# Optimization experiments

Measured on AMD Instinct MI355X. Metric: run time of the kernel, lower is better.

The kernel has to match this reference:

```python
import jax, jax.numpy as jnp
import numpy as np

B, LQ, LD, H, C = 128, 32, 512, 768, 128


def setup_inputs() -> dict:
    key = jax.random.key(0)
    ks = jax.random.split(key, 8)
    return {
        "query_hidden": jax.random.normal(ks[0], (B, LQ, H), dtype=jnp.float32),
        "doc_hidden": jax.random.normal(ks[1], (B, LD, H), dtype=jnp.float32),
        "query_mask": jax.random.randint(ks[2], (B, LQ), 0, 2, dtype=jnp.int32),
        "doc_mask": jax.random.randint(ks[3], (B, LD), 0, 2, dtype=jnp.int32),
        "W_comp": jax.random.normal(ks[4], (H, C), dtype=jnp.float32) * (1.0 / np.sqrt(H)),
        "b_comp": jax.random.normal(ks[5], (C,), dtype=jnp.float32) * 0.02,
        "w_stop": jax.random.normal(ks[6], (C, 1), dtype=jnp.float32) * (1.0 / np.sqrt(C)),
        "b_stop": jnp.ones((1,), dtype=jnp.float32),  # nn.init.constant_(bias, 1)
        "score_merger": jnp.zeros((1,), dtype=jnp.float32),
    }


def reference(query_hidden, doc_hidden, query_mask, doc_mask,
              W_comp, b_comp, w_stop, b_stop, score_merger):
    qm = query_mask.astype(bool)  # [B, LQ]
    dm = doc_mask.astype(bool)    # [B, LD]

    # encode_shared: CLS vec is the UNcompressed hidden state at position 0
    q_cls = query_hidden[:, 0, :]  # [B, H]
    d_cls = doc_hidden[:, 0, :]    # [B, H]

    # compressor (Linear H->C)
    q_vecs = jnp.einsum('blh,hc->blc', query_hidden, W_comp) + b_comp  # [B, LQ, C]
    d_tok = jnp.einsum('blh,hc->blc', doc_hidden, W_comp) + b_comp     # [B, LD, C]

    # encode_query: zero masked query tokens
    q_vecs = q_vecs * qm[..., None]

    # encode_doc: stopword reducer (relu of Linear C->1), then importance + mask
    importance = jax.nn.relu(jnp.einsum('blc,co->blo', d_tok, w_stop) + b_stop)  # [B, LD, 1]
    d_vecs = d_tok * importance * dm[..., None]

    # CLS score: dot product of (uncompressed) CLS vectors
    cls_score = jnp.sum(q_cls * d_cls, axis=-1)  # [B]

    # term score: MaxSim over doc tokens, masked sum over query tokens
    scores = jnp.einsum('bqc,bkc->bqk', q_vecs, d_vecs)      # [B, LQ, LD]
    scores = jnp.where(dm[:, None, :], scores, -1000.0)
    term = jnp.max(scores, axis=-1)                          # [B, LQ]
    term_score = jnp.sum(jnp.where(qm, term, 0.0), axis=-1)  # [B]

    w = jax.nn.sigmoid(score_merger[0])
    cls_score = cls_score * w
    term_score = term_score * (1.0 - w)
    score = cls_score + term_score
    return (score, cls_score, term_score)
```

## Files before the change

### kernel.cpp

```cpp
#include <hip/hip_runtime.h>
#include <hip/hip_bf16.h>

#define Bb 128
#define LQ 32
#define LD 512
#define Hh 768
#define Cc 128

#define QBLOCKS ((Bb * LQ) / 64)
#define DBLOCKS ((Bb * LD) / 64)

typedef short bf16x8 __attribute__((ext_vector_type(8)));
typedef float f32x4 __attribute__((ext_vector_type(4)));

__device__ __forceinline__ short f2bf(float f) {
  union { float f; unsigned u; } v;
  v.f = f;
  unsigned u = v.u + (0x7FFFu + ((v.u >> 16) & 1u));
  return (short)(u >> 16);
}

__device__ __forceinline__ void pack8(bf16x8& d, const float4& lo, const float4& hi) {
  d[0] = f2bf(lo.x); d[1] = f2bf(lo.y); d[2] = f2bf(lo.z); d[3] = f2bf(lo.w);
  d[4] = f2bf(hi.x); d[5] = f2bf(hi.y); d[6] = f2bf(hi.z); d[7] = f2bf(hi.w);
}

__global__ __launch_bounds__(256) void k_wt(const float* __restrict__ W,
                                            short* __restrict__ Wt) {
  int idx = blockIdx.x * 256 + threadIdx.x;
  int h = idx >> 7;
  int c = idx & 127;
  Wt[c * Hh + h] = f2bf(W[idx]);
}

__global__ __launch_bounds__(256) void k_proj_all(
    const float* __restrict__ qh, const float* __restrict__ dh,
    const short* __restrict__ Wt, const float* __restrict__ bcomp,
    const int* __restrict__ qmask, const int* __restrict__ dmask,
    const float* __restrict__ wstop, const float* __restrict__ bstop,
    float* __restrict__ qv, float* __restrict__ dv) {
  const int tid = threadIdx.x;
  const int wave = tid >> 6;
  const int lane = tid & 63;
  const int quad = lane >> 4;
  const int lm = lane & 15;

  const int blk = blockIdx.x;
  const bool is_doc = blk < DBLOCKS;
  const float* X;
  float* Y;
  const int* mask;
  long row0;
  if (is_doc) {
    X = dh; Y = dv; mask = dmask;
    row0 = (long)blk * 64 + wave * 16;
  } else {
    X = qh; Y = qv; mask = qmask;
    row0 = (long)(blk - DBLOCKS) * 64 + wave * 16;
  }

  const float* pa = X + (row0 + lm) * (long)Hh + quad * 8;
  const short* pb = Wt + lm * Hh + quad * 8;

  f32x4 acc[8];
#pragma unroll
  for (int j = 0; j < 8; ++j) acc[j] = (f32x4){0.f, 0.f, 0.f, 0.f};

  float4 c0 = *(const float4*)(pa);
  float4 c1 = *(const float4*)(pa + 4);
  float4 c2 = *(const float4*)(pa + 32);
  float4 c3 = *(const float4*)(pa + 36);

  for (int kk = 0; kk < Hh; kk += 64) {
    int kn = kk + 64;
    if (kn >= Hh) kn = 0;
    float4 n0 = *(const float4*)(pa + kn);
    float4 n1 = *(const float4*)(pa + kn + 4);
    float4 n2 = *(const float4*)(pa + kn + 32);
    float4 n3 = *(const float4*)(pa + kn + 36);

    bf16x8 fa;
    pack8(fa, c0, c1);
#pragma unroll
    for (int j = 0; j < 8; ++j) {
      bf16x8 fb = *(const bf16x8*)(pb + j * 16 * Hh + kk);
      acc[j] = __builtin_amdgcn_mfma_f32_16x16x32_bf16(fa, fb, acc[j], 0, 0, 0);
    }
    pack8(fa, c2, c3);
#pragma unroll
    for (int j = 0; j < 8; ++j) {
      bf16x8 fb = *(const bf16x8*)(pb + j * 16 * Hh + kk + 32);
      acc[j] = __builtin_amdgcn_mfma_f32_16x16x32_bf16(fa, fb, acc[j], 0, 0, 0);
    }
    c0 = n0; c1 = n1; c2 = n2; c3 = n3;
  }

  float bc[8], wsv[8];
#pragma unroll
  for (int j = 0; j < 8; ++j) bc[j] = bcomp[j * 16 + lm];
  if (is_doc) {
#pragma unroll
    for (int j = 0; j < 8; ++j) wsv[j] = wstop[j * 16 + lm];
  }
  const float bs = is_doc ? bstop[0] : 0.f;

#pragma unroll
  for (int r = 0; r < 4; ++r) {
    const long row = row0 + quad * 4 + r;
    float v[8];
#pragma unroll
    for (int j = 0; j < 8; ++j) v[j] = acc[j][r] + bc[j];
    float scale;
    if (is_doc) {
      float p = 0.f;
#pragma unroll
      for (int j = 0; j < 8; ++j) p += v[j] * wsv[j];
      p += __shfl_xor(p, 1);
      p += __shfl_xor(p, 2);
      p += __shfl_xor(p, 4);
      p += __shfl_xor(p, 8);
      float imp = fmaxf(p + bs, 0.f);
      scale = imp * (float)mask[row];
    } else {
      scale = (float)mask[row];
    }
    float* yr = Y + row * Cc;
#pragma unroll
    for (int j = 0; j < 8; ++j) yr[j * 16 + lm] = v[j] * scale;
  }
}

__global__ __launch_bounds__(256) void k_scores(
    const float* __restrict__ Qv, const float* __restrict__ Dv,
    const int* __restrict__ dmask, float* __restrict__ partial) {
  const int chunk = blockIdx.x;
  const int b = blockIdx.y;
  const int tid = threadIdx.x;
  __shared__ float lq[LQ][Cc + 4];
  __shared__ float ldv[64][Cc + 4];
  __shared__ float pm[LQ][16];
  __shared__ int dmsk[64];

  {
    const float4* src = (const float4*)(Qv + (size_t)b * LQ * Cc);
    for (int i = tid; i < LQ * Cc / 4; i += 256) {
      float4 v = src[i];
      int q = i >> 5;
      int c = (i & 31) << 2;
      *(float4*)&lq[q][c] = v;
    }
  }
  const int k0 = chunk * 64;
  {
    const float4* src = (const float4*)(Dv + ((size_t)b * LD + k0) * Cc);
    for (int i = tid; i < 64 * Cc / 4; i += 256) {
      float4 v = src[i];
      int k = i >> 5;
      int c = (i & 31) << 2;
      *(float4*)&ldv[k][c] = v;
    }
  }
  if (tid < 64) dmsk[tid] = dmask[(size_t)b * LD + k0 + tid];
  __syncthreads();

  const int qt = tid & 15;
  const int kt = tid >> 4;
  const int kbase = kt * 4;
  float a[2][4];
#pragma unroll
  for (int qi = 0; qi < 2; ++qi)
#pragma unroll
    for (int ki = 0; ki < 4; ++ki) a[qi][ki] = 0.f;

  for (int c = 0; c < Cc; c += 4) {
    float4 q0 = *(float4*)&lq[qt][c];
    float4 q1 = *(float4*)&lq[qt + 16][c];
    float4 d0 = *(float4*)&ldv[kbase + 0][c];
    float4 d1 = *(float4*)&ldv[kbase + 1][c];
    float4 d2 = *(float4*)&ldv[kbase + 2][c];
    float4 d3 = *(float4*)&ldv[kbase + 3][c];
    a[0][0] += q0.x * d0.x + q0.y * d0.y + q0.z * d0.z + q0.w * d0.w;
    a[0][1] += q0.x * d1.x + q0.y * d1.y + q0.z * d1.z + q0.w * d1.w;
    a[0][2] += q0.x * d2.x + q0.y * d2.y + q0.z * d2.z + q0.w * d2.w;
    a[0][3] += q0.x * d3.x + q0.y * d3.y + q0.z * d3.z + q0.w * d3.w;
    a[1][0] += q1.x * d0.x + q1.y * d0.y + q1.z * d0.z + q1.w * d0.w;
    a[1][1] += q1.x * d1.x + q1.y * d1.y + q1.z * d1.z + q1.w * d1.w;
    a[1][2] += q1.x * d2.x + q1.y * d2.y + q1.z * d2.z + q1.w * d2.w;
    a[1][3] += q1.x * d3.x + q1.y * d3.y + q1.z * d3.z + q1.w * d3.w;
  }
  float m0 = -1000.f, m1 = -1000.f;
#pragma unroll
  for (int ki = 0; ki < 4; ++ki) {
    if (dmsk[kbase + ki]) {
      m0 = fmaxf(m0, a[0][ki]);
      m1 = fmaxf(m1, a[1][ki]);
    }
  }
  pm[qt][kt] = m0;
  pm[qt + 16][kt] = m1;
  __syncthreads();
  if (tid < LQ) {
    float mx = pm[tid][0];
#pragma unroll
    for (int t = 1; t < 16; ++t) mx = fmaxf(mx, pm[tid][t]);
    partial[((size_t)b * LQ + tid) * 8 + chunk] = mx;
  }
}

__global__ __launch_bounds__(256) void k_final(
    const float* __restrict__ qh, const float* __restrict__ dh,
    const int* __restrict__ qmask, const float* __restrict__ partial,
    const float* __restrict__ merger, float* __restrict__ out) {
  const int b = blockIdx.x;
  const int tid = threadIdx.x;
  __shared__ float red[256];
  __shared__ float clss;
  const float* qc = qh + (size_t)b * LQ * Hh;
  const float* dc = dh + (size_t)b * LD * Hh;
  float s = 0.f;
  for (int h = tid; h < Hh; h += 256) s += qc[h] * dc[h];
  red[tid] = s;
  __syncthreads();
  for (int off = 128; off > 0; off >>= 1) {
    if (tid < off) red[tid] += red[tid + off];
    __syncthreads();
  }
  if (tid == 0) clss = red[0];
  __syncthreads();
  float t = 0.f;
  if (tid < LQ) {
    const float* pp = partial + ((size_t)b * LQ + tid) * 8;
    float mx = pp[0];
#pragma unroll
    for (int c = 1; c < 8; ++c) mx = fmaxf(mx, pp[c]);
    if (qmask[b * LQ + tid]) t = mx;
  }
  red[tid] = t;
  __syncthreads();
  for (int off = 128; off > 0; off >>= 1) {
    if (tid < off) red[tid] += red[tid + off];
    __syncthreads();
  }
  if (tid == 0) {
    float w = 1.f / (1.f + expf(-merger[0]));
    float cs = clss * w;
    float ts = red[0] * (1.f - w);
    out[b] = cs + ts;
    out[Bb + b] = cs;
    out[2 * Bb + b] = ts;
  }
}

extern "C" void kernel_launch(void* const* d_in, const int* in_sizes, int n_in,
                              void* d_out, int out_size, void* d_ws, size_t ws_size,
                              hipStream_t stream) {
  const float* qh  = (const float*)d_in[0];
  const float* dh  = (const float*)d_in[1];
  const int*   qm  = (const int*)d_in[2];
  const int*   dm  = (const int*)d_in[3];
  const float* W   = (const float*)d_in[4];
  const float* bc  = (const float*)d_in[5];
  const float* wst = (const float*)d_in[6];
  const float* bst = (const float*)d_in[7];
  const float* mrg = (const float*)d_in[8];
  float* out = (float*)d_out;

  char* ws = (char*)d_ws;
  short* Wt  = (short*)ws;
  float* qv  = (float*)(ws + 196608);
  float* dv  = (float*)(ws + 196608 + 2097152);
  float* prt = (float*)(ws + 196608 + 2097152 + 33554432);

  k_wt<<<(Hh * Cc) / 256, 256, 0, stream>>>(W, Wt);
  k_proj_all<<<DBLOCKS + QBLOCKS, 256, 0, stream>>>(qh, dh, Wt, bc, qm, dm,
                                                    wst, bst, qv, dv);
  k_scores<<<dim3(8, Bb), 256, 0, stream>>>(qv, dv, dm, prt);
  k_final<<<Bb, 256, 0, stream>>>(qh, dh, qm, prt, mrg, out);
}
```

Baseline: 395.8 us.

## Stage projection A and B tiles through LDS via direct global-to-LDS loads

```diff
diff --git a/kernel.cpp b/kernel.cpp
--- a/kernel.cpp
+++ b/kernel.cpp
@@ -23,6 +23,12 @@
 __device__ __forceinline__ void pack8(bf16x8& d, const float4& lo, const float4& hi) {
   d[0] = f2bf(lo.x); d[1] = f2bf(lo.y); d[2] = f2bf(lo.z); d[3] = f2bf(lo.w);
   d[4] = f2bf(hi.x); d[5] = f2bf(hi.y); d[6] = f2bf(hi.z); d[7] = f2bf(hi.w);
+}
+
+__device__ __forceinline__ void gload16(const void* g, void* l) {
+  __builtin_amdgcn_global_load_lds(
+      (const __attribute__((address_space(1))) void*)g,
+      (__attribute__((address_space(3))) void*)l, 16, 0, 0);
 }
 
 __global__ __launch_bounds__(256) void k_wt(const float* __restrict__ W,
@@ -39,6 +45,9 @@
     const int* __restrict__ qmask, const int* __restrict__ dmask,
     const float* __restrict__ wstop, const float* __restrict__ bstop,
     float* __restrict__ qv, float* __restrict__ dv) {
+  __shared__ float lA[64 * 64];
+  __shared__ short lB[128 * 64];
+
   const int tid = threadIdx.x;
   const int wave = tid >> 6;
   const int lane = tid & 63;
@@ -50,51 +59,61 @@
   const float* X;
   float* Y;
   const int* mask;
-  long row0;
+  long row0b;
   if (is_doc) {
     X = dh; Y = dv; mask = dmask;
-    row0 = (long)blk * 64 + wave * 16;
+    row0b = (long)blk * 64;
   } else {
     X = qh; Y = qv; mask = qmask;
-    row0 = (long)(blk - DBLOCKS) * 64 + wave * 16;
-  }
-
-  const float* pa = X + (row0 + lm) * (long)Hh + quad * 8;
-  const short* pb = Wt + lm * Hh + quad * 8;
+    row0b = (long)(blk - DBLOCKS) * 64;
+  }
 
   f32x4 acc[8];
 #pragma unroll
   for (int j = 0; j < 8; ++j) acc[j] = (f32x4){0.f, 0.f, 0.f, 0.f};
 
-  float4 c0 = *(const float4*)(pa);
-  float4 c1 = *(const float4*)(pa + 4);
-  float4 c2 = *(const float4*)(pa + 32);
-  float4 c3 = *(const float4*)(pa + 36);
+  const int ubase = wave * 256 + lane;
 
   for (int kk = 0; kk < Hh; kk += 64) {
-    int kn = kk + 64;
-    if (kn >= Hh) kn = 0;
-    float4 n0 = *(const float4*)(pa + kn);
-    float4 n1 = *(const float4*)(pa + kn + 4);
-    float4 n2 = *(const float4*)(pa + kn + 32);
-    float4 n3 = *(const float4*)(pa + kn + 36);
-
-    bf16x8 fa;
-    pack8(fa, c0, c1);
-#pragma unroll
-    for (int j = 0; j < 8; ++j) {
-      bf16x8 fb = *(const bf16x8*)(pb + j * 16 * Hh + kk);
-      acc[j] = __builtin_amdgcn_mfma_f32_16x16x32_bf16(fa, fb, acc[j], 0, 0, 0);
-    }
-    pack8(fa, c2, c3);
-#pragma unroll
-    for (int j = 0; j < 8; ++j) {
-      bf16x8 fb = *(const bf16x8*)(pb + j * 16 * Hh + kk + 32);
-      acc[j] = __builtin_amdgcn_mfma_f32_16x16x32_bf16(fa, fb, acc[j], 0, 0, 0);
-    }
-    c0 = n0; c1 = n1; c2 = n2; c3 = n3;
-  }
-
+#pragma unroll
+    for (int i = 0; i < 4; ++i) {
+      int u = ubase + i * 64;
+      int r = u >> 4, s = u & 15;
+      int g = s ^ (r & 7);
+      gload16(X + (row0b + r) * (long)Hh + kk + g * 4,
+              &lA[(wave * 4 + i) * 256]);
+    }
+#pragma unroll
+    for (int i = 0; i < 4; ++i) {
+      int u = ubase + i * 64;
+      int n = u >> 3, s = u & 7;
+      int g = s ^ (n & 7);
+      gload16(Wt + n * Hh + kk + g * 8,
+              &lB[(wave * 4 + i) * 512]);
+    }
+    __syncthreads();
+
+    const int rr = wave * 16 + lm;
+#pragma unroll
+    for (int h = 0; h < 2; ++h) {
+      const int gf = h * 8 + quad * 2;
+      const int s0 = gf ^ (lm & 7);
+      const int s1 = (gf + 1) ^ (lm & 7);
+      float4 a0 = *(const float4*)&lA[rr * 64 + s0 * 4];
+      float4 a1 = *(const float4*)&lA[rr * 64 + s1 * 4];
+      bf16x8 fa;
+      pack8(fa, a0, a1);
+      const int sb = (h * 4 + quad) ^ (lm & 7);
+#pragma unroll
+      for (int j = 0; j < 8; ++j) {
+        bf16x8 fb = *(const bf16x8*)&lB[(j * 16 + lm) * 64 + sb * 8];
+        acc[j] = __builtin_amdgcn_mfma_f32_16x16x32_bf16(fa, fb, acc[j], 0, 0, 0);
+      }
+    }
+    __syncthreads();
+  }
+
+  const long row0 = row0b + wave * 16;
   float bc[8], wsv[8];
 #pragma unroll
   for (int j = 0; j < 8; ++j) bc[j] = bcomp[j * 16 + lm];
```

After: 345.9 us. 12.6% less time.

## Stage projection GEMM tiles through double-buffered LDS with 128-row blocks

Applied to the files above, without the earlier changes.

```diff
diff --git a/kernel.cpp b/kernel.cpp
--- a/kernel.cpp
+++ b/kernel.cpp
@@ -7,10 +7,11 @@
 #define Hh 768
 #define Cc 128
 
-#define QBLOCKS ((Bb * LQ) / 64)
-#define DBLOCKS ((Bb * LD) / 64)
+#define DBLOCKS ((Bb * LD) / 128)
+#define QBLOCKS ((Bb * LQ) / 128)
 
 typedef short bf16x8 __attribute__((ext_vector_type(8)));
+typedef short bf16x4 __attribute__((ext_vector_type(4)));
 typedef float f32x4 __attribute__((ext_vector_type(4)));
 
 __device__ __forceinline__ short f2bf(float f) {
@@ -18,11 +19,6 @@
   v.f = f;
   unsigned u = v.u + (0x7FFFu + ((v.u >> 16) & 1u));
   return (short)(u >> 16);
-}
-
-__device__ __forceinline__ void pack8(bf16x8& d, const float4& lo, const float4& hi) {
-  d[0] = f2bf(lo.x); d[1] = f2bf(lo.y); d[2] = f2bf(lo.z); d[3] = f2bf(lo.w);
-  d[4] = f2bf(hi.x); d[5] = f2bf(hi.y); d[6] = f2bf(hi.z); d[7] = f2bf(hi.w);
 }
 
 __global__ __launch_bounds__(256) void k_wt(const float* __restrict__ W,
@@ -33,14 +29,20 @@
   Wt[c * Hh + h] = f2bf(W[idx]);
 }
 
-__global__ __launch_bounds__(256) void k_proj_all(
+__global__ __launch_bounds__(512) void k_proj_all(
     const float* __restrict__ qh, const float* __restrict__ dh,
     const short* __restrict__ Wt, const float* __restrict__ bcomp,
     const int* __restrict__ qmask, const int* __restrict__ dmask,
     const float* __restrict__ wstop, const float* __restrict__ bstop,
     float* __restrict__ qv, float* __restrict__ dv) {
+  constexpr int ASTR = 144;
+  constexpr int BSTR = 160;
+  constexpr int ASZ = 128 * ASTR;
+  constexpr int BSZ = 128 * BSTR;
+  __shared__ __align__(16) char sm[2][ASZ + BSZ];
+
   const int tid = threadIdx.x;
-  const int wave = tid >> 6;
+  const int w = tid >> 6;
   const int lane = tid & 63;
   const int quad = lane >> 4;
   const int lm = lane & 15;
@@ -50,51 +52,67 @@
   const float* X;
   float* Y;
   const int* mask;
-  long row0;
+  long row0b;
   if (is_doc) {
     X = dh; Y = dv; mask = dmask;
-    row0 = (long)blk * 64 + wave * 16;
+    row0b = (long)blk * 128;
   } else {
     X = qh; Y = qv; mask = qmask;
-    row0 = (long)(blk - DBLOCKS) * 64 + wave * 16;
-  }
-
-  const float* pa = X + (row0 + lm) * (long)Hh + quad * 8;
-  const short* pb = Wt + lm * Hh + quad * 8;
+    row0b = (long)(blk - DBLOCKS) * 128;
+  }
+
+  const float* gA = X + (row0b + w * 16 + (lane >> 4)) * (long)Hh + (lane & 15) * 4;
+  const short* gB = Wt + (w * 16 + (lane >> 3)) * Hh + (lane & 7) * 8;
+  const int aoff = (w * 16 + (lane >> 4)) * ASTR + (lane & 15) * 8;
+  const int boff = (w * 16 + (lane >> 3)) * BSTR + (lane & 7) * 16;
 
   f32x4 acc[8];
 #pragma unroll
   for (int j = 0; j < 8; ++j) acc[j] = (f32x4){0.f, 0.f, 0.f, 0.f};
 
-  float4 c0 = *(const float4*)(pa);
-  float4 c1 = *(const float4*)(pa + 4);
-  float4 c2 = *(const float4*)(pa + 32);
-  float4 c3 = *(const float4*)(pa + 36);
-
-  for (int kk = 0; kk < Hh; kk += 64) {
-    int kn = kk + 64;
-    if (kn >= Hh) kn = 0;
-    float4 n0 = *(const float4*)(pa + kn);
-    float4 n1 = *(const float4*)(pa + kn + 4);
-    float4 n2 = *(const float4*)(pa + kn + 32);
-    float4 n3 = *(const float4*)(pa + kn + 36);
-
-    bf16x8 fa;
-    pack8(fa, c0, c1);
-#pragma unroll
-    for (int j = 0; j < 8; ++j) {
-      bf16x8 fb = *(const bf16x8*)(pb + j * 16 * Hh + kk);
-      acc[j] = __builtin_amdgcn_mfma_f32_16x16x32_bf16(fa, fb, acc[j], 0, 0, 0);
-    }
-    pack8(fa, c2, c3);
-#pragma unroll
-    for (int j = 0; j < 8; ++j) {
-      bf16x8 fb = *(const bf16x8*)(pb + j * 16 * Hh + kk + 32);
-      acc[j] = __builtin_amdgcn_mfma_f32_16x16x32_bf16(fa, fb, acc[j], 0, 0, 0);
-    }
-    c0 = n0; c1 = n1; c2 = n2; c3 = n3;
-  }
-
+  float4 ar[4];
+  bf16x8 br[2];
+#pragma unroll
+  for (int i = 0; i < 4; ++i) ar[i] = *(const float4*)(gA + i * 4 * Hh);
+#pragma unroll
+  for (int i = 0; i < 2; ++i) br[i] = *(const bf16x8*)(gB + i * 8 * Hh);
+
+  for (int kk = 0; kk < Hh / 64; ++kk) {
+    char* bufA = sm[kk & 1];
+    char* bufB = sm[kk & 1] + ASZ;
+
+#pragma unroll
+    for (int i = 0; i < 4; ++i) {
+      bf16x4 p;
+      p[0] = f2bf(ar[i].x); p[1] = f2bf(ar[i].y);
+      p[2] = f2bf(ar[i].z); p[3] = f2bf(ar[i].w);
+      *(bf16x4*)(bufA + aoff + i * 4 * ASTR) = p;
+    }
+#pragma unroll
+    for (int i = 0; i < 2; ++i)
+      *(bf16x8*)(bufB + boff + i * 8 * BSTR) = br[i];
+    __syncthreads();
+
+    if (kk + 1 < Hh / 64) {
+      const long go = (long)(kk + 1) * 64;
+#pragma unroll
+      for (int i = 0; i < 4; ++i) ar[i] = *(const float4*)(gA + i * 4 * Hh + go);
+#pragma unroll
+      for (int i = 0; i < 2; ++i) br[i] = *(const bf16x8*)(gB + i * 8 * Hh + go);
+    }
+
+#pragma unroll
+    for (int ks = 0; ks < 2; ++ks) {
+      bf16x8 fa = *(const bf16x8*)(bufA + (w * 16 + lm) * ASTR + ks * 64 + quad * 16);
+#pragma unroll
+      for (int j = 0; j < 8; ++j) {
+        bf16x8 fb = *(const bf16x8*)(bufB + (j * 16 + lm) * BSTR + ks * 64 + quad * 16);
+        acc[j] = __builtin_amdgcn_mfma_f32_16x16x32_bf16(fa, fb, acc[j], 0, 0, 0);
+      }
+    }
+  }
+
+  const long row0 = row0b + w * 16;
   float bc[8], wsv[8];
 #pragma unroll
   for (int j = 0; j < 8; ++j) bc[j] = bcomp[j * 16 + lm];
@@ -272,7 +290,7 @@
   float* prt = (float*)(ws + 196608 + 2097152 + 33554432);
 
   k_wt<<<(Hh * Cc) / 256, 256, 0, stream>>>(W, Wt);
-  k_proj_all<<<DBLOCKS + QBLOCKS, 256, 0, stream>>>(qh, dh, Wt, bc, qm, dm,
+  k_proj_all<<<DBLOCKS + QBLOCKS, 512, 0, stream>>>(qh, dh, Wt, bc, qm, dm,
                                                     wst, bst, qv, dv);
   k_scores<<<dim3(8, Bb), 256, 0, stream>>>(qv, dv, dm, prt);
   k_final<<<Bb, 256, 0, stream>>>(qh, dh, qm, prt, mrg, out);
```

Result: faster. 343.7 us (-13.2%).
